# Kernel optimization log

Hardware: AMD Instinct MI355X
Metric: run time of the kernel (lower is better)

## Reference

```python
import jax, jax.numpy as jnp
from jax import lax
import numpy as np


def setup_inputs() -> dict:
    key = jax.random.key(0)
    im = jax.random.normal(key, (16, 3, 1024, 1024), dtype=jnp.float32)
    return {"im": im, "levels": 4}


def _pyr_reduce(x, kern):
    # replicate-pad by 2 on each spatial side (matches the torch.cat edge copies)
    xp = jnp.pad(x, ((0, 0), (0, 0), (2, 2), (2, 2)), mode="edge")
    # original: valid 5x5 conv then [0::2, 0::2] slice == stride-2 valid conv
    # depthwise over the 3 channels (same kernel each channel)
    return lax.conv_general_dilated(
        xp, kern,
        window_strides=(2, 2), padding="VALID",
        dimension_numbers=("NCHW", "OIHW", "NCHW"),
        feature_group_count=3,
    )


def reference(im, levels):
    kvec = jnp.array([0.0625, 0.25, 0.375, 0.25, 0.0625], dtype=im.dtype)
    k2 = jnp.outer(kvec, kvec)                       # kernel1 = kernelv * kernelh
    kern = jnp.broadcast_to(k2, (3, 1, 5, 5))        # depthwise OIHW
    gpyr = [im]
    for _ in range(levels - 1):
        gpyr.append(_pyr_reduce(gpyr[-1], kern))
    return tuple(gpyr)
```

## Files before the change

kernel.cpp:

```cpp
#include <hip/hip_runtime.h>


__device__ __forceinline__ float S(bool l, bool r, float L, float I, float R) {
    return l ? L : (r ? R : I);
}
__device__ __forceinline__ float4 S4(bool l, bool r, float4 L, float4 I, float4 R) {
    float4 o;
    o.x = S(l, r, L.x, I.x, R.x);
    o.y = S(l, r, L.y, I.y, R.y);
    o.z = S(l, r, L.z, I.z, R.z);
    o.w = S(l, r, L.w, I.w, R.w);
    return o;
}

template <bool FUSE>
__global__ __launch_bounds__(256) void gpyr_reduce(const float* __restrict__ in,
                                                   float* __restrict__ out0,
                                                   float* __restrict__ out1,
                                                   int Hin, int Win, int Hout, int Wout) {
    const int ox0 = (blockIdx.x * blockDim.x + threadIdx.x) * 4;
    const int oy  = blockIdx.y * blockDim.y + threadIdx.y;
    const int img = blockIdx.z;
    if (ox0 >= Wout || oy >= Hout) return;

    const float k0 = 0.0625f, k1 = 0.25f, k2 = 0.375f;
    const float kk[5] = {k0, k1, k2, k1, k0};

    const bool left  = (ox0 == 0);
    const bool right = (2 * ox0 + 12 > Win);
    int xb = 2 * ox0 - 4;
    if (left)  xb = 0;
    if (right) xb = Win - 16;

    const float* ip = in + (size_t)img * Hin * Win;

    float v[11];
#pragma unroll
    for (int i = 0; i < 11; ++i) v[i] = 0.0f;

    float4 cp0A, cp0B, cp1A, cp1B;

#pragma unroll
    for (int ky = 0; ky < 5; ++ky) {
        int iy = 2 * oy + ky - 2;
        iy = min(max(iy, 0), Hin - 1);
        const float4* rp4 = (const float4*)(ip + (size_t)iy * Win + xb);
        float4 A = rp4[0], B = rp4[1], C = rp4[2], D = rp4[3];

        if (FUSE && ky == 2) { cp0A = S4(left, right, A, B, C); cp0B = S4(left, right, B, C, D); }
        if (FUSE && ky == 3) { cp1A = S4(left, right, A, B, C); cp1B = S4(left, right, B, C, D); }

        const float w = kk[ky];
        v[0]  += w * S(left, right, A.x, A.z, B.z);
        v[1]  += w * S(left, right, A.x, A.w, B.w);
        v[2]  += w * S(left, right, A.x, B.x, C.x);
        v[3]  += w * S(left, right, A.y, B.y, C.y);
        v[4]  += w * S(left, right, A.z, B.z, C.z);
        v[5]  += w * S(left, right, A.w, B.w, C.w);
        v[6]  += w * S(left, right, B.x, C.x, D.x);
        v[7]  += w * S(left, right, B.y, C.y, D.y);
        v[8]  += w * S(left, right, B.z, C.z, D.z);
        v[9]  += w * S(left, right, B.w, C.w, D.w);
        v[10] += w * S(left, right, C.x, D.x, D.w);
    }

    if (FUSE) {
        float* op = out0 + (size_t)img * Hin * Win + (size_t)(2 * oy) * Win + 2 * ox0;
        *(float4*)(op)           = cp0A;
        *(float4*)(op + 4)       = cp0B;
        *(float4*)(op + Win)     = cp1A;
        *(float4*)(op + Win + 4) = cp1B;
    }

    float4 o;
    o.x = k0 * v[0] + k1 * v[1] + k2 * v[2] + k1 * v[3] + k0 * v[4];
    o.y = k0 * v[2] + k1 * v[3] + k2 * v[4] + k1 * v[5] + k0 * v[6];
    o.z = k0 * v[4] + k1 * v[5] + k2 * v[6] + k1 * v[7] + k0 * v[8];
    o.w = k0 * v[6] + k1 * v[7] + k2 * v[8] + k1 * v[9] + k0 * v[10];

    *(float4*)(out1 + (size_t)img * Hout * Wout + (size_t)oy * Wout + ox0) = o;
}

extern "C" void kernel_launch(void* const* d_in, const int* in_sizes, int n_in,
                              void* d_out, int out_size, void* d_ws, size_t ws_size,
                              hipStream_t stream) {
    const float* im = (const float*)d_in[0];
    float* out = (float*)d_out;

    const int NC = 16 * 3;
    const size_t L0 = (size_t)NC * 1024 * 1024;
    const size_t L1 = (size_t)NC * 512 * 512;
    const size_t L2 = (size_t)NC * 256 * 256;

    float* out0 = out;
    float* out1 = out0 + L0;
    float* out2 = out1 + L1;
    float* out3 = out2 + L2;

    auto cfg = [](int Wout, int Hout, dim3& block, dim3& grid) {
        int tpx = Wout / 4; if (tpx > 64) tpx = 64;
        int tpy = 256 / tpx;
        block = dim3(tpx, tpy, 1);
        grid = dim3((Wout / 4 + tpx - 1) / tpx, (Hout + tpy - 1) / tpy, 16 * 3);
    };

    {
        dim3 block, grid;
        cfg(512, 512, block, grid);
        gpyr_reduce<true><<<grid, block, 0, stream>>>(im, out0, out1, 1024, 1024, 512, 512);
    }
    {
        dim3 block, grid;
        cfg(256, 256, block, grid);
        gpyr_reduce<false><<<grid, block, 0, stream>>>(out1, nullptr, out2, 512, 512, 256, 256);
    }
    {
        dim3 block, grid;
        cfg(128, 128, block, grid);
        gpyr_reduce<false><<<grid, block, 0, stream>>>(out2, nullptr, out3, 256, 256, 128, 128);
    }
}
```

Measured before the change: 140.6 us.

## Stage input tiles in LDS and compute two output rows per thread

Adds an LDS-tiled reduce kernel that loads a 19-row by 520-column halo tile once per block, then has each thread produce two output rows from seven shared rows. This removes the redundant global loads of the five-row vertical window. The level-0 copy is written out from LDS as well. The last level keeps the old direct-load kernel. The trade-offs are about 40KB of LDS per block, which limits occupancy, plus a block barrier.

```diff
diff --git a/kernel.cpp b/kernel.cpp
--- a/kernel.cpp
+++ b/kernel.cpp
@@ -1,23 +1,111 @@
 #include <hip/hip_runtime.h>
 
 
-__device__ __forceinline__ float S(bool l, bool r, float L, float I, float R) {
+__global__ __launch_bounds__(256) void gpyr_reduce_old(
+        const float* __restrict__ in, float* __restrict__ out,
+        int Hin, int Win, int Hout, int Wout);
+
+template <bool FUSE>
+__global__ __launch_bounds__(256) void gpyr_reduce_lds(
+        const float* __restrict__ in,
+        float* __restrict__ out0,
+        float* __restrict__ out1,
+        int Hin, int Win, int Hout, int Wout) {
+    __shared__ float lds[19][520];
+
+    const int X   = blockIdx.x * 256;
+    const int Y   = blockIdx.y * 8;
+    const int img = blockIdx.z;
+    const int tid = threadIdx.y * 64 + threadIdx.x;
+
+    const float* ip = in + (size_t)img * Hin * Win;
+
+    for (int idx = tid; idx < 19 * 130; idx += 256) {
+        const int r  = idx / 130;
+        const int c4 = idx % 130;
+        const int iy = min(max(2 * Y - 2 + r, 0), Hin - 1);
+        const int gx = 2 * X - 4 + 4 * c4;
+        const float* rowp = ip + (size_t)iy * Win;
+        float4 val;
+        if (gx >= 0 && gx + 4 <= Win) {
+            val = *(const float4*)(rowp + gx);
+        } else {
+            val.x = rowp[min(max(gx + 0, 0), Win - 1)];
+            val.y = rowp[min(max(gx + 1, 0), Win - 1)];
+            val.z = rowp[min(max(gx + 2, 0), Win - 1)];
+            val.w = rowp[min(max(gx + 3, 0), Win - 1)];
+        }
+        *(float4*)&lds[r][4 * c4] = val;
+    }
+    __syncthreads();
+
+    if (FUSE) {
+        float* op = out0 + (size_t)img * Hin * Win;
+        for (int idx = tid; idx < 16 * 128; idx += 256) {
+            const int r  = idx / 128;
+            const int c4 = idx % 128;
+            float4 val = *(const float4*)&lds[2 + r][4 + 4 * c4];
+            *(float4*)(op + (size_t)(2 * Y + r) * Win + 2 * X + 4 * c4) = val;
+        }
+    }
+
+    const int tx = threadIdx.x, ty = threadIdx.y;
+    const float k0 = 0.0625f, k1 = 0.25f, k2 = 0.375f;
+    const float kk[5] = {k0, k1, k2, k1, k0};
+
+    float v0[11], v1[11];
+#pragma unroll
+    for (int i = 0; i < 11; ++i) { v0[i] = 0.0f; v1[i] = 0.0f; }
+
+#pragma unroll
+    for (int s = 0; s < 7; ++s) {
+        const float* lp = &lds[4 * ty + s][8 * tx];
+        float4 A = *(const float4*)(lp);
+        float4 B = *(const float4*)(lp + 4);
+        float4 C = *(const float4*)(lp + 8);
+        float4 D = *(const float4*)(lp + 12);
+        const float x0 = A.z, x1 = A.w, x2 = B.x, x3 = B.y, x4 = B.z, x5 = B.w,
+                    x6 = C.x, x7 = C.y, x8 = C.z, x9 = C.w, x10 = D.x;
+        if (s <= 4) {
+            const float w = kk[s];
+            v0[0] += w * x0; v0[1] += w * x1; v0[2] += w * x2; v0[3] += w * x3;
+            v0[4] += w * x4; v0[5] += w * x5; v0[6] += w * x6; v0[7] += w * x7;
+            v0[8] += w * x8; v0[9] += w * x9; v0[10] += w * x10;
+        }
+        if (s >= 2) {
+            const float w = kk[s - 2];
+            v1[0] += w * x0; v1[1] += w * x1; v1[2] += w * x2; v1[3] += w * x3;
+            v1[4] += w * x4; v1[5] += w * x5; v1[6] += w * x6; v1[7] += w * x7;
+            v1[8] += w * x8; v1[9] += w * x9; v1[10] += w * x10;
+        }
+    }
+
+    float* o1p = out1 + (size_t)img * Hout * Wout;
+    {
+        float4 o;
+        o.x = k0 * v0[0] + k1 * v0[1] + k2 * v0[2] + k1 * v0[3] + k0 * v0[4];
+        o.y = k0 * v0[2] + k1 * v0[3] + k2 * v0[4] + k1 * v0[5] + k0 * v0[6];
+        o.z = k0 * v0[4] + k1 * v0[5] + k2 * v0[6] + k1 * v0[7] + k0 * v0[8];
+        o.w = k0 * v0[6] + k1 * v0[7] + k2 * v0[8] + k1 * v0[9] + k0 * v0[10];
+        *(float4*)(o1p + (size_t)(Y + 2 * ty) * Wout + X + 4 * tx) = o;
+    }
+    {
+        float4 o;
+        o.x = k0 * v1[0] + k1 * v1[1] + k2 * v1[2] + k1 * v1[3] + k0 * v1[4];
+        o.y = k0 * v1[2] + k1 * v1[3] + k2 * v1[4] + k1 * v1[5] + k0 * v1[6];
+        o.z = k0 * v1[4] + k1 * v1[5] + k2 * v1[6] + k1 * v1[7] + k0 * v1[8];
+        o.w = k0 * v1[6] + k1 * v1[7] + k2 * v1[8] + k1 * v1[9] + k0 * v1[10];
+        *(float4*)(o1p + (size_t)(Y + 2 * ty + 1) * Wout + X + 4 * tx) = o;
+    }
+}
+
+__device__ __forceinline__ float Ssel(bool l, bool r, float L, float I, float R) {
     return l ? L : (r ? R : I);
 }
-__device__ __forceinline__ float4 S4(bool l, bool r, float4 L, float4 I, float4 R) {
-    float4 o;
-    o.x = S(l, r, L.x, I.x, R.x);
-    o.y = S(l, r, L.y, I.y, R.y);
-    o.z = S(l, r, L.z, I.z, R.z);
-    o.w = S(l, r, L.w, I.w, R.w);
-    return o;
-}
 
-template <bool FUSE>
-__global__ __launch_bounds__(256) void gpyr_reduce(const float* __restrict__ in,
-                                                   float* __restrict__ out0,
-                                                   float* __restrict__ out1,
-                                                   int Hin, int Win, int Hout, int Wout) {
+__global__ __launch_bounds__(256) void gpyr_reduce_old(
+        const float* __restrict__ in, float* __restrict__ out,
+        int Hin, int Win, int Hout, int Wout) {
     const int ox0 = (blockIdx.x * blockDim.x + threadIdx.x) * 4;
     const int oy  = blockIdx.y * blockDim.y + threadIdx.y;
     const int img = blockIdx.z;
@@ -38,38 +126,24 @@
 #pragma unroll
     for (int i = 0; i < 11; ++i) v[i] = 0.0f;
 
-    float4 cp0A, cp0B, cp1A, cp1B;
-
 #pragma unroll
     for (int ky = 0; ky < 5; ++ky) {
         int iy = 2 * oy + ky - 2;
         iy = min(max(iy, 0), Hin - 1);
         const float4* rp4 = (const float4*)(ip + (size_t)iy * Win + xb);
         float4 A = rp4[0], B = rp4[1], C = rp4[2], D = rp4[3];
-
-        if (FUSE && ky == 2) { cp0A = S4(left, right, A, B, C); cp0B = S4(left, right, B, C, D); }
-        if (FUSE && ky == 3) { cp1A = S4(left, right, A, B, C); cp1B = S4(left, right, B, C, D); }
-
         const float w = kk[ky];
-        v[0]  += w * S(left, right, A.x, A.z, B.z);
-        v[1]  += w * S(left, right, A.x, A.w, B.w);
-        v[2]  += w * S(left, right, A.x, B.x, C.x);
-        v[3]  += w * S(left, right, A.y, B.y, C.y);
-        v[4]  += w * S(left, right, A.z, B.z, C.z);
-        v[5]  += w * S(left, right, A.w, B.w, C.w);
-        v[6]  += w * S(left, right, B.x, C.x, D.x);
-        v[7]  += w * S(left, right, B.y, C.y, D.y);
-        v[8]  += w * S(left, right, B.z, C.z, D.z);
-        v[9]  += w * S(left, right, B.w, C.w, D.w);
-        v[10] += w * S(left, right, C.x, D.x, D.w);
-    }
-
-    if (FUSE) {
-        float* op = out0 + (size_t)img * Hin * Win + (size_t)(2 * oy) * Win + 2 * ox0;
-        *(float4*)(op)           = cp0A;
-        *(float4*)(op + 4)       = cp0B;
-        *(float4*)(op + Win)     = cp1A;
-        *(float4*)(op + Win + 4) = cp1B;
+        v[0]  += w * Ssel(left, right, A.x, A.z, B.z);
+        v[1]  += w * Ssel(left, right, A.x, A.w, B.w);
+        v[2]  += w * Ssel(left, right, A.x, B.x, C.x);
+        v[3]  += w * Ssel(left, right, A.y, B.y, C.y);
+        v[4]  += w * Ssel(left, right, A.z, B.z, C.z);
+        v[5]  += w * Ssel(left, right, A.w, B.w, C.w);
+        v[6]  += w * Ssel(left, right, B.x, C.x, D.x);
+        v[7]  += w * Ssel(left, right, B.y, C.y, D.y);
+        v[8]  += w * Ssel(left, right, B.z, C.z, D.z);
+        v[9]  += w * Ssel(left, right, B.w, C.w, D.w);
+        v[10] += w * Ssel(left, right, C.x, D.x, D.w);
     }
 
     float4 o;
@@ -78,7 +152,7 @@
     o.z = k0 * v[4] + k1 * v[5] + k2 * v[6] + k1 * v[7] + k0 * v[8];
     o.w = k0 * v[6] + k1 * v[7] + k2 * v[8] + k1 * v[9] + k0 * v[10];
 
-    *(float4*)(out1 + (size_t)img * Hout * Wout + (size_t)oy * Wout + ox0) = o;
+    *(float4*)(out + (size_t)img * Hout * Wout + (size_t)oy * Wout + ox0) = o;
 }
 
 extern "C" void kernel_launch(void* const* d_in, const int* in_sizes, int n_in,
@@ -97,26 +171,19 @@
     float* out2 = out1 + L1;
     float* out3 = out2 + L2;
 
-    auto cfg = [](int Wout, int Hout, dim3& block, dim3& grid) {
-        int tpx = Wout / 4; if (tpx > 64) tpx = 64;
-        int tpy = 256 / tpx;
-        block = dim3(tpx, tpy, 1);
-        grid = dim3((Wout / 4 + tpx - 1) / tpx, (Hout + tpy - 1) / tpy, 16 * 3);
-    };
-
     {
-        dim3 block, grid;
-        cfg(512, 512, block, grid);
-        gpyr_reduce<true><<<grid, block, 0, stream>>>(im, out0, out1, 1024, 1024, 512, 512);
+        dim3 block(64, 4, 1);
+        dim3 grid(512 / 256, 512 / 8, NC);
+        gpyr_reduce_lds<true><<<grid, block, 0, stream>>>(im, out0, out1, 1024, 1024, 512, 512);
     }
     {
-        dim3 block, grid;
-        cfg(256, 256, block, grid);
-        gpyr_reduce<false><<<grid, block, 0, stream>>>(out1, nullptr, out2, 512, 512, 256, 256);
+        dim3 block(64, 4, 1);
+        dim3 grid(256 / 256, 256 / 8, NC);
+        gpyr_reduce_lds<false><<<grid, block, 0, stream>>>(out1, nullptr, out2, 512, 512, 256, 256);
     }
     {
-        dim3 block, grid;
-        cfg(128, 128, block, grid);
-        gpyr_reduce<false><<<grid, block, 0, stream>>>(out2, nullptr, out3, 256, 256, 128, 128);
+        dim3 block(32, 8, 1);
+        dim3 grid(1, 16, NC);
+        gpyr_reduce_old<<<grid, block, 0, stream>>>(out2, out3, 256, 256, 128, 128);
     }
 }
```

Result: no change. 142.7 us (+1.5%).
